# Optimization experiments

Hardware: AMD Instinct MI355X
Metric: run time of the kernel (lower is better)

Reference implementation:

```python
import jax, jax.numpy as jnp
import numpy as np


def setup_inputs() -> dict:
    key = jax.random.key(0)
    ks = jax.random.split(key, 8)
    B, N, D = 8, 2048, 128
    s = 1.0 / float(np.sqrt(D))
    node = jax.random.normal(ks[0], (B, N, D), dtype=jnp.float32)
    node_mask = jax.random.randint(ks[1], (B, N), 0, 2, dtype=jnp.int32)
    punctuation_graph = jax.random.randint(ks[2], (B, N, N), 0, 2, dtype=jnp.int32)
    w_nw = jax.random.uniform(ks[3], (1, D), jnp.float32, -s, s)
    b_nw = jax.random.uniform(ks[4], (1,), jnp.float32, -s, s)
    w_self = jax.random.uniform(ks[5], (D, D), jnp.float32, -s, s)
    b_self = jax.random.uniform(ks[6], (D,), jnp.float32, -s, s)
    w_punct = jax.random.uniform(ks[7], (D, D), jnp.float32, -s, s)
    return {"node": node, "node_mask": node_mask, "punctuation_graph": punctuation_graph,
            "w_nw": w_nw, "b_nw": b_nw, "w_self": w_self, "b_self": b_self,
            "w_punct": w_punct, "iteration_steps": 2}


def reference(node, node_mask, punctuation_graph, w_nw, b_nw, w_self, b_self, w_punct, iteration_steps):
    B, N, D = node.shape
    # dd_graph = mask outer product with zeroed diagonal; graph = dd_graph * punctuation_graph
    eye = jnp.eye(N, dtype=punctuation_graph.dtype)
    dd = node_mask[:, None, :] * node_mask[:, :, None] * (1 - eye)[None, :, :]  # [B,N,N]
    graph = dd * punctuation_graph  # [B,N,N] int, binary
    nbr_num = graph.sum(-1)  # [B,N]
    # replace_masked_values(nbr_num, nbr_num>=1, 1): nodes with no neighbors get denom 1
    nbr_f = jnp.where(nbr_num >= 1, nbr_num.astype(node.dtype), jnp.asarray(1.0, node.dtype))
    gmask = graph > 0
    weights = []
    x = node
    for _ in range(iteration_steps):  # small fixed step count
        dw = jax.nn.sigmoid(jnp.einsum('bnd,od->bno', x, w_nw) + b_nw)[..., 0]  # [B,N]
        weights.append(dw)
        self_info = jnp.einsum('bnd,ed->bne', x, w_self) + b_self  # [B,N,D]
        info_p = jnp.einsum('bnd,ed->bne', x, w_punct)  # [B,N,D]
        # node_weight[b,i,j] = dw[b,j] where graph[b,i,j] else 0
        nw = jnp.where(gmask, dw[:, None, :], jnp.asarray(0.0, x.dtype))  # [B,N,N]
        agg = jnp.einsum('bnm,bmd->bnd', nw, info_p) / nbr_f[..., None]
        x = jax.nn.relu(self_info + agg)
    all_weight = jnp.stack(weights, axis=1)  # [B, steps, N]
    return x, all_weight
```

## Files before the change

kernel.cpp:

```cpp
#include <hip/hip_runtime.h>
#include <hip/hip_bf16.h>

#define BB 8
#define NN 2048
#define DD 128

typedef __attribute__((ext_vector_type(8))) __bf16 bf16x8;
typedef __attribute__((ext_vector_type(4))) float f32x4;
typedef __attribute__((ext_vector_type(4))) int   i32x4;

static __device__ __forceinline__ unsigned short f2bf(float f) {
    union { float f; unsigned u; } v; v.f = f;
    unsigned r = (v.u + 0x7FFFu + ((v.u >> 16) & 1u)) >> 16;
    return (unsigned short)r;
}
static __device__ __forceinline__ float bf2f(unsigned short b) {
    union { unsigned u; float f; } v; v.u = ((unsigned)b) << 16;
    return v.f;
}

__global__ __launch_bounds__(256) void kernP3(
    const int* __restrict__ punct, const int* __restrict__ mask,
    const float* __restrict__ w_self, const float* __restrict__ w_punct,
    unsigned* __restrict__ pk, float* __restrict__ scale_g, float* __restrict__ pdm_g,
    unsigned short* __restrict__ wsb, unsigned short* __restrict__ wpb)
{
    const int bid = blockIdx.x;
    const int t = threadIdx.x;

    if (bid >= 2048) {
        const int cb = bid - 2048;
        const float* src = (cb < 8) ? w_self : w_punct;
        unsigned short* dst = (cb < 8) ? wsb : wpb;
        const size_t i0 = (size_t)(cb & 7) * 2048 + (size_t)t * 8;
        f32x4 a = *(const f32x4*)(src + i0);
        f32x4 c = *(const f32x4*)(src + i0 + 4);
        unsigned q0 = f2bf(a.x) | ((unsigned)f2bf(a.y) << 16);
        unsigned q1 = f2bf(a.z) | ((unsigned)f2bf(a.w) << 16);
        unsigned q2 = f2bf(c.x) | ((unsigned)f2bf(c.y) << 16);
        unsigned q3 = f2bf(c.z) | ((unsigned)f2bf(c.w) << 16);
        i32x4 pw = {(int)q0, (int)q1, (int)q2, (int)q3};
        *(i32x4*)(dst + i0) = pw;
        return;
    }

    const int wave = t >> 6, lane = t & 63;
    const int row0 = bid * 8 + wave * 2;
    const int b = row0 >> 11;
    const int* mrow = mask + (size_t)b * NN;

    unsigned mw = 0;
    #pragma unroll
    for (int q = 0; q < 8; ++q) {
        i32x4 m = *(const i32x4*)(mrow + lane * 32 + q * 4);
        unsigned nib = (m.x & 1) | ((m.y & 1) << 1) | ((m.z & 1) << 2) | ((m.w & 1) << 3);
        mw |= nib << (4 * q);
    }

    #pragma unroll
    for (int r = 0; r < 2; ++r) {
        const int row = row0 + r;
        const int i = row & (NN - 1);
        const int mi = mrow[i];
        if (mi == 0) {
            if (lane == 0) { scale_g[row] = 0.f; pdm_g[row] = 0.f; }
            continue;
        }
        const int* prow = punct + (size_t)row * NN;
        i32x4 v[8];
        #pragma unroll
        for (int q = 0; q < 8; ++q)
            v[q] = *(const i32x4*)(prow + lane * 32 + q * 4);
        unsigned wd = 0;
        #pragma unroll
        for (int q = 0; q < 8; ++q) {
            unsigned nib = (v[q].x & 1) | ((v[q].y & 1) << 1)
                         | ((v[q].z & 1) << 2) | ((v[q].w & 1) << 3);
            wd |= nib << (4 * q);
        }
        wd &= mw;
        pk[(size_t)row * 64 + lane] = wd;

        int acc = __popc(wd);
        if ((i >> 5) == lane) acc += (int)((wd >> (i & 31)) & 1u) << 16;
        #pragma unroll
        for (int o = 32; o > 0; o >>= 1) acc += __shfl_xor(acc, o, 64);
        if (lane == 0) {
            const int nall = acc & 0xFFFF;
            const int pd   = acc >> 16;
            const int nbr  = nall - pd;
            scale_g[row] = 1.f / (float)(nbr < 1 ? 1 : nbr);
            pdm_g[row]   = (float)pd;
        }
    }
}

static __device__ __forceinline__ void kernB_body(
    int n0, const float* __restrict__ x,
    const float* __restrict__ w_nw,  const float* __restrict__ b_nw,
    const unsigned short* __restrict__ wsb, const float* __restrict__ b_self,
    const unsigned short* __restrict__ wpb,
    float* __restrict__ si_out,
    unsigned short* __restrict__ yne_out,
    unsigned short* __restrict__ yT_out,
    float* __restrict__ aw_out)
{
    __shared__ unsigned short xt[64*32];
    __shared__ unsigned short wst[128*32];
    __shared__ unsigned short wpt[128*32];
    __shared__ float wnw_l[DD];
    __shared__ float red[256];
    __shared__ float dw_l[64];
    __shared__ unsigned short ytl[128*72];

    const int t  = threadIdx.x;
    const int b  = n0 >> 11;
    const int nb = n0 & (NN - 1);

    if (t < DD) wnw_l[t] = w_nw[t];
    __syncthreads();

    const int wave = t >> 6, lane = t & 63;
    const int wm = wave >> 1, wn = wave & 1;
    const int quad = lane >> 4, l16 = lane & 15;

    const int n_loc = t >> 2, dq = t & 3;
    const int we = t >> 1,   wh = t & 1;

    f32x4 accs[2][4] = {}; f32x4 accp[2][4] = {};
    float dwpart = 0.f;

    #pragma unroll
    for (int kk = 0; kk < 4; ++kk) {
        const int k0 = kk * 32;
        {
            const float* xs = x + (size_t)(n0 + n_loc) * DD + k0 + dq * 8;
            f32x4 a = *(const f32x4*)xs;
            f32x4 c = *(const f32x4*)(xs + 4);
            const float* wv = &wnw_l[k0 + dq * 8];
            dwpart += a.x*wv[0] + a.y*wv[1] + a.z*wv[2] + a.w*wv[3]
                    + c.x*wv[4] + c.y*wv[5] + c.z*wv[6] + c.w*wv[7];
            unsigned q0 = f2bf(a.x) | ((unsigned)f2bf(a.y) << 16);
            unsigned q1 = f2bf(a.z) | ((unsigned)f2bf(a.w) << 16);
            unsigned q2 = f2bf(c.x) | ((unsigned)f2bf(c.y) << 16);
            unsigned q3 = f2bf(c.z) | ((unsigned)f2bf(c.w) << 16);
            i32x4 pw = {(int)q0,(int)q1,(int)q2,(int)q3};
            *(i32x4*)&xt[n_loc*32 + dq*8] = pw;
        }
        {
            const unsigned short* s1 = wsb + (size_t)we * DD + k0 + wh*16;
            const unsigned short* s2 = wpb + (size_t)we * DD + k0 + wh*16;
            i32x4 a0 = *(const i32x4*)s1;
            i32x4 a1 = *(const i32x4*)(s1 + 8);
            *(i32x4*)&wst[we*32 + wh*16]     = a0;
            *(i32x4*)&wst[we*32 + wh*16 + 8] = a1;
            i32x4 c0 = *(const i32x4*)s2;
            i32x4 c1 = *(const i32x4*)(s2 + 8);
            *(i32x4*)&wpt[we*32 + wh*16]     = c0;
            *(i32x4*)&wpt[we*32 + wh*16 + 8] = c1;
        }
        __syncthreads();
        bf16x8 af[2], bs[4], bp[4];
        #pragma unroll
        for (int mt = 0; mt < 2; ++mt)
            af[mt] = *(const bf16x8*)&xt[(wm*32 + mt*16 + l16)*32 + quad*8];
        #pragma unroll
        for (int nt = 0; nt < 4; ++nt) {
            const int er = wn*64 + nt*16 + l16;
            bs[nt] = *(const bf16x8*)&wst[er*32 + quad*8];
            bp[nt] = *(const bf16x8*)&wpt[er*32 + quad*8];
        }
        #pragma unroll
        for (int mt = 0; mt < 2; ++mt)
            #pragma unroll
            for (int nt = 0; nt < 4; ++nt) {
                accs[mt][nt] = __builtin_amdgcn_mfma_f32_16x16x32_bf16(af[mt], bs[nt], accs[mt][nt], 0, 0, 0);
                accp[mt][nt] = __builtin_amdgcn_mfma_f32_16x16x32_bf16(af[mt], bp[nt], accp[mt][nt], 0, 0, 0);
            }
        __syncthreads();
    }

    red[t] = dwpart;
    __syncthreads();
    if (t < 64) {
        float s = red[4*t] + red[4*t+1] + red[4*t+2] + red[4*t+3] + b_nw[0];
        float dv = 1.f / (1.f + __expf(-s));
        dw_l[t] = dv;
        aw_out[(size_t)b * 2 * NN + nb + t] = dv;
    }
    __syncthreads();

    #pragma unroll
    for (int mt = 0; mt < 2; ++mt) {
        #pragma unroll
        for (int nt = 0; nt < 4; ++nt) {
            const int e = wn*64 + nt*16 + l16;
            const float bsv = b_self[e];
            #pragma unroll
            for (int r = 0; r < 4; ++r) {
                const int nl = wm*32 + mt*16 + quad*4 + r;
                const size_t idx = (size_t)(n0 + nl) * DD + e;
                si_out[idx] = accs[mt][nt][r] + bsv;
                const float yv = dw_l[nl] * accp[mt][nt][r];
                const unsigned short ub = f2bf(yv);
                yne_out[idx] = ub;
                ytl[e*72 + nl] = ub;
            }
        }
    }
    __syncthreads();
    {
        const int e = t >> 1, half = t & 1;
        const i32x4* src = (const i32x4*)&ytl[e*72 + half*32];
        i32x4 v0 = src[0], v1 = src[1], v2 = src[2], v3 = src[3];
        i32x4* dst = (i32x4*)(yT_out + (size_t)(b*DD + e) * NN + nb + half*32);
        dst[0] = v0; dst[1] = v1; dst[2] = v2; dst[3] = v3;
    }
}

__global__ __launch_bounds__(256) void kernB(
    const float* __restrict__ x,
    const unsigned short* __restrict__ wsb, const unsigned short* __restrict__ wpb,
    const float* __restrict__ w_nw, const float* __restrict__ b_nw,
    const float* __restrict__ b_self,
    float* __restrict__ si, unsigned short* __restrict__ yne,
    unsigned short* __restrict__ yT, float* __restrict__ aw_s)
{
    kernB_body(blockIdx.x * 64, x, w_nw, b_nw, wsb, b_self, wpb,
               si, yne, yT, aw_s);
}

__global__ __launch_bounds__(128) void kernC3(
    const unsigned* __restrict__ pk,
    const float* __restrict__ scale_g, const float* __restrict__ pdm_g,
    const unsigned short* __restrict__ yT,
    const float* __restrict__ si,
    const unsigned short* __restrict__ yne,
    float* __restrict__ x_out)
{
    __shared__ unsigned pPk[32 * 68];
    __shared__ float scale_l[32];
    __shared__ float pdm_l[32];

    const int t   = threadIdx.x;
    const int b   = blockIdx.x & 7;
    const int idx = blockIdx.x >> 3;
    const int i0  = (idx >> 1) * 32;
    const int e0  = (idx & 1) * 64;
    const size_t rg0 = (size_t)b * NN + i0;

    #pragma unroll
    for (int r = 0; r < 4; ++r) {
        const int u   = r * 128 + t;
        const int row = u >> 4;
        const int wq  = (u & 15) * 4;
        i32x4 v = *(const i32x4*)(pk + (rg0 + row) * 64 + wq);
        *(i32x4*)&pPk[row * 68 + wq] = v;
    }
    if (t < 32) {
        scale_l[t] = scale_g[rg0 + t];
        pdm_l[t]   = pdm_g[rg0 + t];
    }
    __syncthreads();

    const int wn = t >> 6, lane = t & 63;
    const int quad = lane >> 4, l16 = lane & 15;
    const unsigned short* yTb = yT + (size_t)b * DD * NN;

    f32x4 acc[2][2] = {};

    #pragma unroll 4
    for (int kk = 0; kk < 64; ++kk) {
        bf16x8 bfr[2];
        #pragma unroll
        for (int nt = 0; nt < 2; ++nt) {
            const int e = e0 + wn*32 + nt*16 + l16;
            bfr[nt] = *(const bf16x8*)(yTb + (size_t)e * NN + kk*32 + quad*8);
        }
        bf16x8 af[2];
        #pragma unroll
        for (int mt = 0; mt < 2; ++mt) {
            const unsigned w = pPk[(mt*16 + l16) * 68 + kk];
            const unsigned by = (w >> (quad * 8)) & 0xFFu;
            i32x4 ex;
            ex.x = ((by &   1u) ? 0x3F80 : 0) | ((by &   2u) ? 0x3F800000 : 0);
            ex.y = ((by &   4u) ? 0x3F80 : 0) | ((by &   8u) ? 0x3F800000 : 0);
            ex.z = ((by &  16u) ? 0x3F80 : 0) | ((by &  32u) ? 0x3F800000 : 0);
            ex.w = ((by &  64u) ? 0x3F80 : 0) | ((by & 128u) ? 0x3F800000 : 0);
            union { i32x4 i; bf16x8 h; } cv; cv.i = ex;
            af[mt] = cv.h;
        }
        #pragma unroll
        for (int mt = 0; mt < 2; ++mt)
            #pragma unroll
            for (int nt = 0; nt < 2; ++nt)
                acc[mt][nt] = __builtin_amdgcn_mfma_f32_16x16x32_bf16(af[mt], bfr[nt], acc[mt][nt], 0, 0, 0);
    }

    #pragma unroll
    for (int mt = 0; mt < 2; ++mt) {
        #pragma unroll
        for (int nt = 0; nt < 2; ++nt) {
            const int e = e0 + wn*32 + nt*16 + l16;
            #pragma unroll
            for (int r = 0; r < 4; ++r) {
                const int row = mt*16 + quad*4 + r;
                const size_t idx2 = (rg0 + row) * DD + e;
                const float yv = bf2f(yne[idx2]);
                float v = si[idx2] + scale_l[row] * (acc[mt][nt][r] - pdm_l[row] * yv);
                x_out[idx2] = fmaxf(v, 0.f);
            }
        }
    }
}

extern "C" void kernel_launch(void* const* d_in, const int* in_sizes, int n_in,
                              void* d_out, int out_size, void* d_ws, size_t ws_size,
                              hipStream_t stream) {
    const float* node   = (const float*)d_in[0];
    const int*   mask   = (const int*)  d_in[1];
    const int*   punct  = (const int*)  d_in[2];
    const float* w_nw   = (const float*)d_in[3];
    const float* b_nw   = (const float*)d_in[4];
    const float* w_self = (const float*)d_in[5];
    const float* b_self = (const float*)d_in[6];
    const float* w_punct= (const float*)d_in[7];

    float* xout = (float*)d_out;
    float* aw   = xout + (size_t)BB * NN * DD;

    char* w = (char*)d_ws;
    float*          si   = (float*)w;
    unsigned short* yne  = (unsigned short*)(w + (8u  << 20));
    unsigned short* yT   = (unsigned short*)(w + (12u << 20));
    unsigned*       pk   = (unsigned*)(w + (16u << 20));
    float*          scl  = (float*)(w + (20u << 20));
    float*          pdm  = (float*)(w + (20u << 20) + (64u << 10));
    unsigned short* wsb  = (unsigned short*)(w + (21u << 20));
    unsigned short* wpb  = (unsigned short*)(w + (21u << 20) + (32u << 10));

    kernP3<<<dim3(2064), dim3(256), 0, stream>>>(punct, mask, w_self, w_punct,
                                                 pk, scl, pdm, wsb, wpb);
    kernB <<<dim3(256),  dim3(256), 0, stream>>>(node, wsb, wpb, w_nw, b_nw,
                                                 b_self, si, yne, yT, aw);
    kernC3<<<dim3(1024), dim3(128), 0, stream>>>(pk, scl, pdm, yT, si, yne, xout);
    kernB <<<dim3(256),  dim3(256), 0, stream>>>(xout, wsb, wpb, w_nw, b_nw,
                                                 b_self, si, yne, yT, aw + NN);
    kernC3<<<dim3(1024), dim3(128), 0, stream>>>(pk, scl, pdm, yT, si, yne, xout);
}
```

Before: 294.9 us.

## Fold diagonal correction into self term and retile aggregation with split-K

The producer kernel now folds the diagonal-correction term (scale*pd*y) into the self_info buffer, so the separate bf16 y buffer and its write and reload go away. The aggregation kernel is rewritten to handle 64 rows by all 128 features per block with four waves. Pairs of waves split the K range and reduce through LDS. This cuts redundant graph-bit loads across feature halves and gives more reuse per block, but it uses only 256 blocks and adds an LDS reduction stage. The bit-to-bf16 expansion also switches from selects to multiply tricks.

```diff
diff --git a/kernel.cpp b/kernel.cpp
--- a/kernel.cpp
+++ b/kernel.cpp
@@ -100,8 +100,8 @@
     const float* __restrict__ w_nw,  const float* __restrict__ b_nw,
     const unsigned short* __restrict__ wsb, const float* __restrict__ b_self,
     const unsigned short* __restrict__ wpb,
+    const float* __restrict__ scale_g, const float* __restrict__ pdm_g,
     float* __restrict__ si_out,
-    unsigned short* __restrict__ yne_out,
     unsigned short* __restrict__ yT_out,
     float* __restrict__ aw_out)
 {
@@ -111,6 +111,8 @@
     __shared__ float wnw_l[DD];
     __shared__ float red[256];
     __shared__ float dw_l[64];
+    __shared__ float scl_l[64];
+    __shared__ float pdm_l[64];
     __shared__ unsigned short ytl[128*72];
 
     const int t  = threadIdx.x;
@@ -118,6 +120,8 @@
     const int nb = n0 & (NN - 1);
 
     if (t < DD) wnw_l[t] = w_nw[t];
+    if (t >= 128 && t < 192) { scl_l[t-128] = scale_g[n0 + t - 128]; }
+    if (t >= 192)            { pdm_l[t-192] = pdm_g[n0 + t - 192]; }
     __syncthreads();
 
     const int wave = t >> 6, lane = t & 63;
@@ -200,10 +204,10 @@
             for (int r = 0; r < 4; ++r) {
                 const int nl = wm*32 + mt*16 + quad*4 + r;
                 const size_t idx = (size_t)(n0 + nl) * DD + e;
-                si_out[idx] = accs[mt][nt][r] + bsv;
                 const float yv = dw_l[nl] * accp[mt][nt][r];
                 const unsigned short ub = f2bf(yv);
-                yne_out[idx] = ub;
+                const float yvr = bf2f(ub);
+                si_out[idx] = accs[mt][nt][r] + bsv - scl_l[nl] * pdm_l[nl] * yvr;
                 ytl[e*72 + nl] = ub;
             }
         }
@@ -223,92 +227,100 @@
     const unsigned short* __restrict__ wsb, const unsigned short* __restrict__ wpb,
     const float* __restrict__ w_nw, const float* __restrict__ b_nw,
     const float* __restrict__ b_self,
-    float* __restrict__ si, unsigned short* __restrict__ yne,
-    unsigned short* __restrict__ yT, float* __restrict__ aw_s)
+    const float* __restrict__ scale_g, const float* __restrict__ pdm_g,
+    float* __restrict__ si, unsigned short* __restrict__ yT,
+    float* __restrict__ aw_s)
 {
     kernB_body(blockIdx.x * 64, x, w_nw, b_nw, wsb, b_self, wpb,
-               si, yne, yT, aw_s);
-}
-
-__global__ __launch_bounds__(128) void kernC3(
+               scale_g, pdm_g, si, yT, aw_s);
+}
+
+__global__ __launch_bounds__(256) void kernC4(
     const unsigned* __restrict__ pk,
-    const float* __restrict__ scale_g, const float* __restrict__ pdm_g,
+    const float* __restrict__ scale_g,
     const unsigned short* __restrict__ yT,
-    const float* __restrict__ si,
-    const unsigned short* __restrict__ yne,
+    const float* __restrict__ sip,
     float* __restrict__ x_out)
 {
-    __shared__ unsigned pPk[32 * 68];
-    __shared__ float scale_l[32];
-    __shared__ float pdm_l[32];
-
-    const int t   = threadIdx.x;
-    const int b   = blockIdx.x & 7;
-    const int idx = blockIdx.x >> 3;
-    const int i0  = (idx >> 1) * 32;
-    const int e0  = (idx & 1) * 64;
+    __shared__ unsigned pPk[64 * 68];
+    __shared__ float scale_l[64];
+    __shared__ f32x4 accL[2][16][64];
+
+    const int t  = threadIdx.x;
+    const int b  = blockIdx.x & 7;
+    const int i0 = (blockIdx.x >> 3) * 64;
     const size_t rg0 = (size_t)b * NN + i0;
 
     #pragma unroll
     for (int r = 0; r < 4; ++r) {
-        const int u   = r * 128 + t;
+        const int u   = r * 256 + t;
         const int row = u >> 4;
         const int wq  = (u & 15) * 4;
         i32x4 v = *(const i32x4*)(pk + (rg0 + row) * 64 + wq);
         *(i32x4*)&pPk[row * 68 + wq] = v;
     }
-    if (t < 32) {
-        scale_l[t] = scale_g[rg0 + t];
-        pdm_l[t]   = pdm_g[rg0 + t];
-    }
-    __syncthreads();
-
-    const int wn = t >> 6, lane = t & 63;
+    if (t < 64) scale_l[t] = scale_g[rg0 + t];
+    __syncthreads();
+
+    const int wave = t >> 6, lane = t & 63;
+    const int kh = wave >> 1, eh = wave & 1;
     const int quad = lane >> 4, l16 = lane & 15;
     const unsigned short* yTb = yT + (size_t)b * DD * NN;
 
-    f32x4 acc[2][2] = {};
+    f32x4 acc[4][4] = {};
 
     #pragma unroll 4
-    for (int kk = 0; kk < 64; ++kk) {
-        bf16x8 bfr[2];
-        #pragma unroll
-        for (int nt = 0; nt < 2; ++nt) {
-            const int e = e0 + wn*32 + nt*16 + l16;
+    for (int ks = 0; ks < 32; ++ks) {
+        const int kk = kh * 32 + ks;
+        bf16x8 bfr[4];
+        #pragma unroll
+        for (int nt = 0; nt < 4; ++nt) {
+            const int e = eh*64 + nt*16 + l16;
             bfr[nt] = *(const bf16x8*)(yTb + (size_t)e * NN + kk*32 + quad*8);
         }
-        bf16x8 af[2];
-        #pragma unroll
-        for (int mt = 0; mt < 2; ++mt) {
+        bf16x8 af[4];
+        #pragma unroll
+        for (int mt = 0; mt < 4; ++mt) {
             const unsigned w = pPk[(mt*16 + l16) * 68 + kk];
             const unsigned by = (w >> (quad * 8)) & 0xFFu;
             i32x4 ex;
-            ex.x = ((by &   1u) ? 0x3F80 : 0) | ((by &   2u) ? 0x3F800000 : 0);
-            ex.y = ((by &   4u) ? 0x3F80 : 0) | ((by &   8u) ? 0x3F800000 : 0);
-            ex.z = ((by &  16u) ? 0x3F80 : 0) | ((by &  32u) ? 0x3F800000 : 0);
-            ex.w = ((by &  64u) ? 0x3F80 : 0) | ((by & 128u) ? 0x3F800000 : 0);
+            ex.x = (int)((((by &   1u) << 7) + ((by &   2u) << 22)) * 0x7Fu);
+            ex.y = (int)((((by &   4u) << 5) + ((by &   8u) << 20)) * 0x7Fu);
+            ex.z = (int)((((by &  16u) << 3) + ((by &  32u) << 18)) * 0x7Fu);
+            ex.w = (int)((((by &  64u) << 1) + ((by & 128u) << 16)) * 0x7Fu);
             union { i32x4 i; bf16x8 h; } cv; cv.i = ex;
             af[mt] = cv.h;
         }
         #pragma unroll
-        for (int mt = 0; mt < 2; ++mt)
-            #pragma unroll
-            for (int nt = 0; nt < 2; ++nt)
+        for (int mt = 0; mt < 4; ++mt)
+            #pragma unroll
+            for (int nt = 0; nt < 4; ++nt)
                 acc[mt][nt] = __builtin_amdgcn_mfma_f32_16x16x32_bf16(af[mt], bfr[nt], acc[mt][nt], 0, 0, 0);
     }
 
-    #pragma unroll
-    for (int mt = 0; mt < 2; ++mt) {
-        #pragma unroll
-        for (int nt = 0; nt < 2; ++nt) {
-            const int e = e0 + wn*32 + nt*16 + l16;
-            #pragma unroll
-            for (int r = 0; r < 4; ++r) {
-                const int row = mt*16 + quad*4 + r;
-                const size_t idx2 = (rg0 + row) * DD + e;
-                const float yv = bf2f(yne[idx2]);
-                float v = si[idx2] + scale_l[row] * (acc[mt][nt][r] - pdm_l[row] * yv);
-                x_out[idx2] = fmaxf(v, 0.f);
+    __syncthreads();
+    if (kh == 1) {
+        #pragma unroll
+        for (int mt = 0; mt < 4; ++mt)
+            #pragma unroll
+            for (int nt = 0; nt < 4; ++nt)
+                accL[eh][mt*4 + nt][lane] = acc[mt][nt];
+    }
+    __syncthreads();
+    if (kh == 0) {
+        #pragma unroll
+        for (int mt = 0; mt < 4; ++mt) {
+            #pragma unroll
+            for (int nt = 0; nt < 4; ++nt) {
+                f32x4 o = accL[eh][mt*4 + nt][lane];
+                const int e = eh*64 + nt*16 + l16;
+                #pragma unroll
+                for (int r = 0; r < 4; ++r) {
+                    const int row = mt*16 + quad*4 + r;
+                    const size_t idx = (rg0 + row) * DD + e;
+                    float v = sip[idx] + scale_l[row] * (acc[mt][nt][r] + o[r]);
+                    x_out[idx] = fmaxf(v, 0.f);
+                }
             }
         }
     }
@@ -331,7 +343,6 @@
 
     char* w = (char*)d_ws;
     float*          si   = (float*)w;
-    unsigned short* yne  = (unsigned short*)(w + (8u  << 20));
     unsigned short* yT   = (unsigned short*)(w + (12u << 20));
     unsigned*       pk   = (unsigned*)(w + (16u << 20));
     float*          scl  = (float*)(w + (20u << 20));
@@ -342,9 +353,9 @@
     kernP3<<<dim3(2064), dim3(256), 0, stream>>>(punct, mask, w_self, w_punct,
                                                  pk, scl, pdm, wsb, wpb);
     kernB <<<dim3(256),  dim3(256), 0, stream>>>(node, wsb, wpb, w_nw, b_nw,
-                                                 b_self, si, yne, yT, aw);
-    kernC3<<<dim3(1024), dim3(128), 0, stream>>>(pk, scl, pdm, yT, si, yne, xout);
+                                                 b_self, scl, pdm, si, yT, aw);
+    kernC4<<<dim3(256),  dim3(256), 0, stream>>>(pk, scl, yT, si, xout);
     kernB <<<dim3(256),  dim3(256), 0, stream>>>(xout, wsb, wpb, w_nw, b_nw,
-                                                 b_self, si, yne, yT, aw + NN);
-    kernC3<<<dim3(1024), dim3(128), 0, stream>>>(pk, scl, pdm, yT, si, yne, xout);
-}
+                                                 b_self, scl, pdm, si, yT, aw + NN);
+    kernC4<<<dim3(256),  dim3(256), 0, stream>>>(pk, scl, yT, si, xout);
+}
```

New measurement: 268.0 us. 9.1% less time.
